# Kernel tuning notes

Hardware: AMD Instinct MI355X
Metric: run time of the kernel (lower is better)

Reference implementation:

```python
import math
import jax, jax.numpy as jnp
import numpy as np

D_MODEL = 1024
NUM_HEADS = 16
HEAD_DIM = D_MODEL // NUM_HEADS
EPS = 1e-8


def setup_inputs() -> dict:
    key = jax.random.key(0)
    ks = jax.random.split(key, 9)
    B, T = 2, 2048
    scale = 1.0 / math.sqrt(D_MODEL)
    return {
        "query": jax.random.normal(ks[0], (B, T, D_MODEL), jnp.float32),
        "key": jax.random.normal(ks[1], (B, T, D_MODEL), jnp.float32),
        "value": jax.random.normal(ks[2], (B, T, D_MODEL), jnp.float32),
        "key_padding_mask": jnp.zeros((B, T), dtype=bool),
        "Wq": jax.random.normal(ks[3], (D_MODEL, D_MODEL), jnp.float32) * scale,
        "Wk": jax.random.normal(ks[4], (D_MODEL, D_MODEL), jnp.float32) * scale,
        "Wv": jax.random.normal(ks[5], (D_MODEL, D_MODEL), jnp.float32) * scale,
        "Wo": jax.random.normal(ks[6], (D_MODEL, D_MODEL), jnp.float32) * scale,
        "s_v": jnp.zeros((NUM_HEADS,), jnp.float32),
        "s_r": jnp.zeros((NUM_HEADS,), jnp.float32),
    }


def _l2norm(x, eps=EPS):
    n = jnp.sqrt(jnp.sum(x * x, axis=-1, keepdims=True))
    return x / jnp.maximum(n, eps)


def _tanh_norm(x, eps=EPS):
    # Reconstructed TanhNorm: bound each head vector by tanh of its L2 norm.
    n = jnp.sqrt(jnp.sum(x * x, axis=-1, keepdims=True))
    return jnp.tanh(n) * x / (n + eps)


def reference(query, key, value, key_padding_mask, Wq, Wk, Wv, Wo, s_v, s_r):
    B, T_q, _ = query.shape
    T_k = key.shape[1]
    H, D = NUM_HEADS, HEAD_DIM

    def proj_split(x, W):  # torch Linear: x @ W.T, then split heads -> (B,H,T,D)
        y = jnp.einsum('btm,dm->btd', x, W)
        return y.reshape(x.shape[0], x.shape[1], H, D).transpose(0, 2, 1, 3)

    q = _l2norm(proj_split(query, Wq))
    k = _l2norm(proj_split(key, Wk))
    v = _l2norm(proj_split(value, Wv))

    sim = jnp.einsum('bhqd,bhkd->bhqk', q, k)  # cosine similarities

    w = jnp.exp(s_v) + 1.0  # (H,) window size per head
    r = jnp.exp(s_r) + 1.0  # (H,) sharpness per head

    # Trim-and-Square: alpha = relu(1 - r*(1 - sim))^2
    alpha = jax.nn.relu(1.0 - r[None, :, None, None] * (1.0 - sim)) ** 2

    # Causal cosine softmask: (H, T_q, T_k)
    rel = (jnp.arange(T_k)[None, :] - jnp.arange(T_q)[:, None]).astype(jnp.float32)
    w_ = w[:, None, None]
    cos_mask = 0.5 * (jnp.cos(jnp.pi * rel[None] / w_) + 1.0)
    in_window = (rel[None] > -w_) & (rel[None] <= 0)
    softmask = cos_mask * in_window.astype(jnp.float32)
    alpha = alpha * softmask[None]

    alpha = jnp.where(key_padding_mask[:, None, None, :], 0.0, alpha)

    out = jnp.einsum('bhqk,bhkd->bhqd', alpha, v)
    out = _tanh_norm(out)
    out = out.transpose(0, 2, 1, 3).reshape(B, T_q, H * D)
    return jnp.einsum('btm,dm->btd', out, Wo)
```

## Files before the change

### kernel.cpp

```cpp
#include <hip/hip_runtime.h>
#include <math.h>

#define D_MODEL 1024
#define NUM_HEADS 16
#define HEAD_DIM 64
#define EPS 1e-8f
#define B_SZ 2
#define T_SZ 2048
#define KEXP 2048

typedef unsigned short ushort_t;
typedef __attribute__((ext_vector_type(8))) short bf16x8;
typedef __attribute__((ext_vector_type(4))) float f32x4;

__device__ __forceinline__ ushort_t f2bf(float f) {
    unsigned u = __float_as_uint(f);
    unsigned r = (u + 0x7FFFu + ((u >> 16) & 1u)) >> 16;
    return (ushort_t)r;
}
__device__ __forceinline__ float bf2f(ushort_t h) {
    return __uint_as_float(((unsigned)h) << 16);
}

__device__ __forceinline__ void gload_lds16(const ushort_t* g, ushort_t* l) {
    __builtin_amdgcn_global_load_lds(
        (const __attribute__((address_space(1))) unsigned int*)g,
        (__attribute__((address_space(3))) unsigned int*)l, 16, 0, 0);
}

__global__ __launch_bounds__(256) void expand7(
    const float* q, const float* k, const float* v,
    const float* wq, const float* wk, const float* wv, const float* wo,
    ushort_t* qe, ushort_t* ke, ushort_t* ve,
    ushort_t* wqe, ushort_t* wke, ushort_t* wve, ushort_t* woe)
{
    const float* in; ushort_t* out; int rows;
    switch (blockIdx.z) {
        case 0: in = q;  out = qe;  rows = 4096; break;
        case 1: in = k;  out = ke;  rows = 4096; break;
        case 2: in = v;  out = ve;  rows = 4096; break;
        case 3: in = wq; out = wqe; rows = 1024; break;
        case 4: in = wk; out = wke; rows = 1024; break;
        case 5: in = wv; out = wve; rows = 1024; break;
        default: in = wo; out = woe; rows = 1024; break;
    }
    const int gid = blockIdx.x * 256 + threadIdx.x;
    const int e = gid * 8;
    if (e >= rows * 1024) return;
    const int row = e >> 10;
    const int kk = e & 1023;

    float x[8];
    *(float4*)&x[0] = *(const float4*)&in[(size_t)row * 1024 + kk];
    *(float4*)&x[4] = *(const float4*)&in[(size_t)row * 1024 + kk + 4];

    union { ushort_t s[8]; uint4 u; } hi, lo;
    #pragma unroll
    for (int i = 0; i < 8; ++i) {
        ushort_t h = f2bf(x[i]);
        hi.s[i] = h;
        lo.s[i] = f2bf(x[i] - bf2f(h));
    }
    ushort_t* dst = out + (size_t)row * KEXP + (kk >> 5) * 64 + (kk & 31);
    *(uint4*)dst        = hi.u;
    *(uint4*)(dst + 32) = lo.u;
}

template<int BN, int WAVES_M, int WAVES_N>
__global__ __launch_bounds__(256) void gemm_split(
    const ushort_t* A0, const ushort_t* B0, float* C0,
    const ushort_t* A1, const ushort_t* B1, float* C1,
    const ushort_t* A2, const ushort_t* B2, float* C2,
    int M, int N)
{
    constexpr int BM = 128;
    constexpr int WAVE_M = BM / WAVES_M;
    constexpr int WAVE_N = BN / WAVES_N;
    constexpr int FM = WAVE_M / 16;
    constexpr int FN = WAVE_N / 16;

    const int gx = gridDim.x, gy = gridDim.y;
    const int nwg = gx * gy * gridDim.z;
    const int lid = blockIdx.x + gx * (blockIdx.y + gy * blockIdx.z);
    const int cpx = nwg >> 3;
    const int swz = (lid & 7) * cpx + (lid >> 3);
    const int bz  = swz / (gx * gy);
    const int rem = swz - bz * gx * gy;
    const int by  = rem / gx;
    const int bx  = rem - by * gx;

    const ushort_t* Ae; const ushort_t* Be; float* C;
    if (bz == 0)      { Ae = A0; Be = B0; C = C0; }
    else if (bz == 1) { Ae = A1; Be = B1; C = C1; }
    else              { Ae = A2; Be = B2; C = C2; }

    __shared__ __align__(16) ushort_t As[BM * 64];
    __shared__ __align__(16) ushort_t Bs[BN * 64];

    const int tid = threadIdx.x;
    const int bm = by * BM;
    const int bn = bx * BN;

    const int rr = tid >> 3;
    const int p  = tid & 7;

    const int wid  = tid >> 6;
    const int wm   = wid / WAVES_N;
    const int wn   = wid % WAVES_N;
    const int lane = tid & 63;
    const int lrow = lane & 15;
    const int lk   = lane >> 4;

    f32x4 acc[FM][FN] = {};

    for (int ks = 0; ks < 32; ++ks) {
        const int kb = ks * 64;
        #pragma unroll
        for (int r = 0; r < BM / 32; ++r) {
            const int row = r * 32 + rr;
            const int s = p ^ (row & 7);
            gload_lds16(Ae + (size_t)(bm + row) * KEXP + kb + s * 8,
                        &As[row * 64 + p * 8]);
        }
        #pragma unroll
        for (int r = 0; r < BN / 32; ++r) {
            const int row = r * 32 + rr;
            const int s = p ^ (row & 7);
            gload_lds16(Be + (size_t)(bn + row) * KEXP + kb + s * 8,
                        &Bs[row * 64 + p * 8]);
        }
        __syncthreads();

        bf16x8 ah[FM], al[FM], bh[FN], bl[FN];
        #pragma unroll
        for (int m = 0; m < FM; ++m) {
            const int row = wm * WAVE_M + m * 16 + lrow;
            const int x = row & 7;
            ah[m] = *(const bf16x8*)&As[row * 64 + ((lk)     ^ x) * 8];
            al[m] = *(const bf16x8*)&As[row * 64 + ((lk + 4) ^ x) * 8];
        }
        #pragma unroll
        for (int n = 0; n < FN; ++n) {
            const int row = wn * WAVE_N + n * 16 + lrow;
            const int x = row & 7;
            bh[n] = *(const bf16x8*)&Bs[row * 64 + ((lk)     ^ x) * 8];
            bl[n] = *(const bf16x8*)&Bs[row * 64 + ((lk + 4) ^ x) * 8];
        }
        #pragma unroll
        for (int m = 0; m < FM; ++m)
            #pragma unroll
            for (int n = 0; n < FN; ++n) {
                acc[m][n] = __builtin_amdgcn_mfma_f32_16x16x32_bf16(ah[m], bh[n], acc[m][n], 0, 0, 0);
                acc[m][n] = __builtin_amdgcn_mfma_f32_16x16x32_bf16(al[m], bh[n], acc[m][n], 0, 0, 0);
                acc[m][n] = __builtin_amdgcn_mfma_f32_16x16x32_bf16(ah[m], bl[n], acc[m][n], 0, 0, 0);
            }
        __syncthreads();
    }

    #pragma unroll
    for (int m = 0; m < FM; ++m)
        #pragma unroll
        for (int j = 0; j < 4; ++j) {
            const int row = bm + wm * WAVE_M + m * 16 + lk * 4 + j;
            float* cr = C + (size_t)row * N + bn + wn * WAVE_N + lrow;
            #pragma unroll
            for (int n = 0; n < FN; ++n)
                cr[n * 16] = acc[m][n][j];
        }
}

__device__ __forceinline__ float wred(float x) {
    #pragma unroll
    for (int off = 32; off; off >>= 1) x += __shfl_xor(x, off);
    return x;
}

__global__ __launch_bounds__(256) void attn_kernel(
    const float* __restrict__ Q, const float* __restrict__ Kp, const float* __restrict__ Vp,
    const int* __restrict__ mask, const float* __restrict__ s_v, const float* __restrict__ s_r,
    ushort_t* __restrict__ Oe)
{
    const int lane = threadIdx.x & 63;
    const int wq = (blockIdx.x * blockDim.x + threadIdx.x) >> 6;
    const int i = wq % T_SZ;
    const int h = (wq / T_SZ) % NUM_HEADS;
    const int b = wq / (T_SZ * NUM_HEADS);

    const float w = expf(s_v[h]) + 1.0f;
    const float r = expf(s_r[h]) + 1.0f;

    const size_t base = (size_t)(b * T_SZ) * D_MODEL + h * HEAD_DIM + lane;

    const float qv = Q[base + (size_t)i * D_MODEL];
    const float qn = qv / fmaxf(sqrtf(wred(qv * qv)), EPS);

    int jmin = i - (int)ceilf(w) + 1;
    if (jmin < 0) jmin = 0;

    float acc = 0.0f;
    for (int j = jmin; j <= i; ++j) {
        const float rel = (float)(j - i);
        if (!(rel > -w)) continue;
        const float kv = Kp[base + (size_t)j * D_MODEL];
        const float kn = kv / fmaxf(sqrtf(wred(kv * kv)), EPS);
        const float sim = wred(qn * kn);
        const float cm = 0.5f * (cosf((float)M_PI * rel / w) + 1.0f);
        const float a1 = fmaxf(1.0f - r * (1.0f - sim), 0.0f);
        float alpha = a1 * a1 * cm;
        if (mask[b * T_SZ + j] != 0) alpha = 0.0f;
        const float vv = Vp[base + (size_t)j * D_MODEL];
        const float vn = vv / fmaxf(sqrtf(wred(vv * vv)), EPS);
        acc += alpha * vn;
    }

    const float n = sqrtf(wred(acc * acc));
    const float o = tanhf(n) * acc / (n + EPS);

    const int row = b * T_SZ + i;
    const int kg  = h * HEAD_DIM + lane;
    ushort_t hi = f2bf(o);
    ushort_t lo = f2bf(o - bf2f(hi));
    ushort_t* dst = Oe + (size_t)row * KEXP + (kg >> 5) * 64 + (kg & 31);
    dst[0]  = hi;
    dst[32] = lo;
}

extern "C" void kernel_launch(void* const* d_in, const int* in_sizes, int n_in,
                              void* d_out, int out_size, void* d_ws, size_t ws_size,
                              hipStream_t stream) {
    const float* query = (const float*)d_in[0];
    const float* key   = (const float*)d_in[1];
    const float* value = (const float*)d_in[2];
    const int*   mask  = (const int*)d_in[3];
    const float* Wq    = (const float*)d_in[4];
    const float* Wk    = (const float*)d_in[5];
    const float* Wv    = (const float*)d_in[6];
    const float* Wo    = (const float*)d_in[7];
    const float* s_v   = (const float*)d_in[8];
    const float* s_r   = (const float*)d_in[9];
    float* out = (float*)d_out;

    const int M = B_SZ * T_SZ;
    const size_t MB = 1u << 20;

    char* ws = (char*)d_ws;
    ushort_t* qe  = (ushort_t*)(ws + 0 * MB);
    ushort_t* ke  = (ushort_t*)(ws + 16 * MB);
    ushort_t* ve  = (ushort_t*)(ws + 32 * MB);
    ushort_t* wqe = (ushort_t*)(ws + 48 * MB);
    ushort_t* wke = (ushort_t*)(ws + 52 * MB);
    ushort_t* wve = (ushort_t*)(ws + 56 * MB);
    ushort_t* woe = (ushort_t*)(ws + 60 * MB);
    float*    qp  = (float*)(ws + 64 * MB);
    float*    kp  = (float*)(ws + 80 * MB);
    float*    vp  = (float*)(ws + 96 * MB);
    ushort_t* aoe = qe;

    dim3 blk(256);

    hipLaunchKernelGGL(expand7, dim3(2048, 1, 7), blk, 0, stream,
                       query, key, value, Wq, Wk, Wv, Wo,
                       qe, ke, ve, wqe, wke, wve, woe);

    hipLaunchKernelGGL((gemm_split<128, 2, 2>), dim3(D_MODEL / 128, M / 128, 3), blk, 0, stream,
                       qe, wqe, qp,
                       ke, wke, kp,
                       ve, wve, vp,
                       M, D_MODEL);

    const int total_waves = B_SZ * NUM_HEADS * T_SZ;
    hipLaunchKernelGGL(attn_kernel, dim3(total_waves / 4), blk, 0, stream,
                       qp, kp, vp, mask, s_v, s_r, aoe);

    hipLaunchKernelGGL((gemm_split<64, 4, 1>), dim3(D_MODEL / 64, M / 128, 1), blk, 0, stream,
                       aoe, woe, out,
                       aoe, woe, out,
                       aoe, woe, out,
                       M, D_MODEL);
}
```

Measured before the change: 170.4 us.

## Double-buffer LDS tiles in the split-bf16 projection GEMM to overlap loads

The GEMM main loop now uses two LDS buffer pairs for A and B. The loads for the next K-slice are issued before the MFMA compute on the current slice, and each iteration processes two slices. The goal is to hide global-to-LDS transfer latency behind matrix-core work instead of stalling at a barrier every step. In exchange, shared-memory use per block doubles, which can lower occupancy.

Result: no change. 169.2 us (-0.7%).

```diff
diff --git a/kernel.cpp b/kernel.cpp
--- a/kernel.cpp
+++ b/kernel.cpp
@@ -94,8 +94,10 @@
     else if (bz == 1) { Ae = A1; Be = B1; C = C1; }
     else              { Ae = A2; Be = B2; C = C2; }
 
-    __shared__ __align__(16) ushort_t As[BM * 64];
-    __shared__ __align__(16) ushort_t Bs[BN * 64];
+    __shared__ __align__(16) ushort_t As0[BM * 64];
+    __shared__ __align__(16) ushort_t As1[BM * 64];
+    __shared__ __align__(16) ushort_t Bs0[BN * 64];
+    __shared__ __align__(16) ushort_t Bs1[BN * 64];
 
     const int tid = threadIdx.x;
     const int bm = by * BM;
@@ -113,38 +115,39 @@
 
     f32x4 acc[FM][FN] = {};
 
-    for (int ks = 0; ks < 32; ++ks) {
+    auto stage = [&](ushort_t* AsP, ushort_t* BsP, int ks) {
         const int kb = ks * 64;
         #pragma unroll
         for (int r = 0; r < BM / 32; ++r) {
             const int row = r * 32 + rr;
             const int s = p ^ (row & 7);
             gload_lds16(Ae + (size_t)(bm + row) * KEXP + kb + s * 8,
-                        &As[row * 64 + p * 8]);
+                        &AsP[row * 64 + p * 8]);
         }
         #pragma unroll
         for (int r = 0; r < BN / 32; ++r) {
             const int row = r * 32 + rr;
             const int s = p ^ (row & 7);
             gload_lds16(Be + (size_t)(bn + row) * KEXP + kb + s * 8,
-                        &Bs[row * 64 + p * 8]);
-        }
-        __syncthreads();
-
+                        &BsP[row * 64 + p * 8]);
+        }
+    };
+
+    auto compute = [&](const ushort_t* AsP, const ushort_t* BsP) {
         bf16x8 ah[FM], al[FM], bh[FN], bl[FN];
         #pragma unroll
         for (int m = 0; m < FM; ++m) {
             const int row = wm * WAVE_M + m * 16 + lrow;
             const int x = row & 7;
-            ah[m] = *(const bf16x8*)&As[row * 64 + ((lk)     ^ x) * 8];
-            al[m] = *(const bf16x8*)&As[row * 64 + ((lk + 4) ^ x) * 8];
+            ah[m] = *(const bf16x8*)&AsP[row * 64 + ((lk)     ^ x) * 8];
+            al[m] = *(const bf16x8*)&AsP[row * 64 + ((lk + 4) ^ x) * 8];
         }
         #pragma unroll
         for (int n = 0; n < FN; ++n) {
             const int row = wn * WAVE_N + n * 16 + lrow;
             const int x = row & 7;
-            bh[n] = *(const bf16x8*)&Bs[row * 64 + ((lk)     ^ x) * 8];
-            bl[n] = *(const bf16x8*)&Bs[row * 64 + ((lk + 4) ^ x) * 8];
+            bh[n] = *(const bf16x8*)&BsP[row * 64 + ((lk)     ^ x) * 8];
+            bl[n] = *(const bf16x8*)&BsP[row * 64 + ((lk + 4) ^ x) * 8];
         }
         #pragma unroll
         for (int m = 0; m < FM; ++m)
@@ -154,6 +157,18 @@
                 acc[m][n] = __builtin_amdgcn_mfma_f32_16x16x32_bf16(al[m], bh[n], acc[m][n], 0, 0, 0);
                 acc[m][n] = __builtin_amdgcn_mfma_f32_16x16x32_bf16(ah[m], bl[n], acc[m][n], 0, 0, 0);
             }
+    };
+
+    stage(As0, Bs0, 0);
+    __syncthreads();
+
+    #pragma unroll 1
+    for (int ks = 0; ks < 32; ks += 2) {
+        if (ks + 1 < 32) stage(As1, Bs1, ks + 1);
+        compute(As0, Bs0);
+        __syncthreads();
+        if (ks + 2 < 32) stage(As0, Bs0, ks + 2);
+        compute(As1, Bs1);
         __syncthreads();
     }
 
```
